# Kernel tuning notes

Hardware: AMD Instinct MI355X
Metric: run time of the kernel (lower is better)

Reference implementation:

```python
import jax, jax.numpy as jnp
import numpy as np

N_CIR, N_DIS, D, H = 585, 88, 128, 8
E_CC, E_DD = 20000, 3000
EPS = 1e-16


def _gcn(x, src, dst, ew, W, b, N):
    # PyG GCNConv: add self-loops (weight 1), symmetric normalization, x @ W, scatter-add, + bias
    loop = jnp.arange(N)
    s = jnp.concatenate([src, loop])
    d = jnp.concatenate([dst, loop])
    w = jnp.concatenate([ew, jnp.ones((N,), ew.dtype)])
    deg = jax.ops.segment_sum(w, d, num_segments=N)
    dinv = jnp.where(deg > 0, jax.lax.rsqrt(deg), 0.0)
    norm = dinv[s] * w * dinv[d]                      # [E+N]
    h = x @ W                                         # [N,D]
    out = jax.ops.segment_sum(h[s] * norm[:, None], d, num_segments=N)
    return out + b


def _gat(x, src, dst, ea, W, a_src, a_dst, a_edge, We, b, N):
    # PyG GATConv(heads=H, concat=False, edge_dim=1): self-loops with mean edge_attr fill,
    # leaky_relu attention logits, segment softmax over destination, mean over heads, + bias
    loop = jnp.arange(N)
    s = jnp.concatenate([src, loop])
    d = jnp.concatenate([dst, loop])
    ea = jnp.concatenate([ea, jnp.broadcast_to(ea.mean(0, keepdims=True), (N, ea.shape[1]))], 0)
    h = (x @ W).reshape(N, H, D)                      # [N,H,D]
    e = (ea @ We).reshape(-1, H, D)                   # [E+N,H,D]
    alpha = (h * a_src).sum(-1)[s] + (h * a_dst).sum(-1)[d] + (e * a_edge).sum(-1)
    alpha = jax.nn.leaky_relu(alpha, 0.2)             # [E+N,H]
    amax = jax.ops.segment_max(alpha, d, num_segments=N)
    ex = jnp.exp(alpha - amax[d])
    den = jax.ops.segment_sum(ex, d, num_segments=N)
    alpha = ex / (den[d] + EPS)
    out = jax.ops.segment_sum(h[s] * alpha[:, :, None], d, num_segments=N)  # [N,H,D]
    return out.mean(1) + b


def _branch(x, edges, mat, gw1, gb1, aw, asrc, adst, aedge, awe, ab, gw2, gb2, N):
    src, dst = edges[0], edges[1]
    ew = mat[src, dst]                                # gather edge weights from dense matrix
    f1 = jax.nn.relu(_gcn(x, src, dst, ew, gw1, gb1, N))
    att = jax.nn.relu(_gat(f1, src, dst, ew[:, None], aw, asrc, adst, aedge, awe, ab, N))
    f2 = jax.nn.relu(_gcn(att, src, dst, ew, gw2, gb2, N))
    return f1, f2


def _cnn(f1, f2, Wk, b):
    # Conv2d(2,256,(128,1)) over [1,2,128,N] == per-node GEMM over (2,128) then view/transpose
    Xv = jnp.stack([f1.T, f2.T])                      # [2,D,N]
    return jnp.einsum('ock,ckn->no', Wk[..., 0], Xv) + b  # [N,256]


def setup_inputs():
    ks = jax.random.split(jax.random.key(0), 24)
    rn = lambda i, sh, s=1.0: jax.random.normal(ks[i], sh, jnp.float32) * s
    w = 0.08  # ~glorot scale for fan-in 128
    return {
        'x_cir': rn(0, (N_CIR, D)),
        'x_dis': rn(1, (N_DIS, D)),
        'cc_matrix': jax.random.uniform(ks[2], (N_CIR, N_CIR), jnp.float32),
        'dd_matrix': jax.random.uniform(ks[3], (N_DIS, N_DIS), jnp.float32),
        'gcn_c1_w': rn(4, (D, D), w), 'gcn_c1_b': jnp.zeros((D,), jnp.float32),
        'gat_c_w': rn(5, (D, H * D), w), 'gat_c_asrc': rn(6, (H, D), w),
        'gat_c_adst': rn(7, (H, D), w), 'gat_c_aedge': rn(8, (H, D), w),
        'gat_c_we': rn(9, (1, H * D), w), 'gat_c_b': jnp.zeros((D,), jnp.float32),
        'gcn_c2_w': rn(10, (D, D), w), 'gcn_c2_b': jnp.zeros((D,), jnp.float32),
        'gcn_d1_w': rn(11, (D, D), w), 'gcn_d1_b': jnp.zeros((D,), jnp.float32),
        'gat_d_w': rn(12, (D, H * D), w), 'gat_d_asrc': rn(13, (H, D), w),
        'gat_d_adst': rn(14, (H, D), w), 'gat_d_aedge': rn(15, (H, D), w),
        'gat_d_we': rn(16, (1, H * D), w), 'gat_d_b': jnp.zeros((D,), jnp.float32),
        'gcn_d2_w': rn(17, (D, D), w), 'gcn_d2_b': jnp.zeros((D,), jnp.float32),
        'conv_c_w': rn(18, (256, 2, D, 1), w), 'conv_c_b': jnp.zeros((256,), jnp.float32),
        'conv_d_w': rn(19, (256, 2, D, 1), w), 'conv_d_b': jnp.zeros((256,), jnp.float32),
        'cc_edges': jax.random.randint(ks[20], (2, E_CC), 0, N_CIR),
        'dd_edges': jax.random.randint(ks[21], (2, E_DD), 0, N_DIS),
    }


def reference(x_cir, x_dis, cc_matrix, dd_matrix,
              gcn_c1_w, gcn_c1_b, gat_c_w, gat_c_asrc, gat_c_adst, gat_c_aedge, gat_c_we, gat_c_b,
              gcn_c2_w, gcn_c2_b,
              gcn_d1_w, gcn_d1_b, gat_d_w, gat_d_asrc, gat_d_adst, gat_d_aedge, gat_d_we, gat_d_b,
              gcn_d2_w, gcn_d2_b,
              conv_c_w, conv_c_b, conv_d_w, conv_d_b,
              cc_edges, dd_edges):
    c1, c2 = _branch(x_cir, cc_edges, cc_matrix, gcn_c1_w, gcn_c1_b, gat_c_w, gat_c_asrc,
                     gat_c_adst, gat_c_aedge, gat_c_we, gat_c_b, gcn_c2_w, gcn_c2_b, N_CIR)
    d1, d2 = _branch(x_dis, dd_edges, dd_matrix, gcn_d1_w, gcn_d1_b, gat_d_w, gat_d_asrc,
                     gat_d_adst, gat_d_aedge, gat_d_we, gat_d_b, gcn_d2_w, gcn_d2_b, N_DIS)
    cir_fea = _cnn(c1, c2, conv_c_w, conv_c_b)        # [585,256]
    dis_fea = _cnn(d1, d2, conv_d_w, conv_d_b)        # [88,256]
    return cir_fea @ dis_fea.T, cir_fea, dis_fea
```

## Files before the change

### kernel.cpp

```cpp
#include <hip/hip_runtime.h>

constexpr int NCIR = 585;
constexpr int NDIS = 88;
constexpr int NT   = NCIR + NDIS;
constexpr int DIM  = 128;
constexpr int NH   = 8;
constexpr int ECC  = 20000;
constexpr int EDD  = 3000;
constexpr int ET   = ECC + EDD;
constexpr int CO   = 256;
constexpr int CAP  = 256;
constexpr int F1C  = (NCIR + 3) / 4;
constexpr int F1D  = (NDIS + 3) / 4;
constexpr int NG   = F1C + F1D;
constexpr int GBK  = (ET + 255) / 256;
constexpr int GEMB = (NT + 1) / 2;

__device__ __forceinline__ int decode_cnt(unsigned raw){
  return (int)(raw >= 0xA0000000u ? raw - 0xAAAAAAAAu : raw);
}

struct P {
  const float *x_c, *x_d, *mat_c, *mat_d;
  const float *g1w_c, *g1b_c, *aw_c, *as_c, *ad_c, *ae_c, *we_c, *ab_c, *g2w_c, *g2b_c;
  const float *g1w_d, *g1b_d, *aw_d, *as_d, *ad_d, *ae_d, *we_d, *ab_d, *g2w_d, *g2b_d;
  const float *cw_c, *cb_c, *cw_d, *cb_d;
  const int *csrc, *cdst, *dsrc, *ddst;
  float *hs, *hd, *h, *f1, *hg, *fill_w, *psc, *psd, *wdeg, *wdall;
  unsigned *cnt;
  int *fill_s;
  float *out_score, *out_cir, *out_dis;
};

__global__ __launch_bounds__(256) void k_gg(P p){
  __shared__ float r0[256], r1[256];
  int b = blockIdx.x, t = threadIdx.x;
  if (b < GBK){
    int e = b * 256 + t;
    float wc = 0.0f, wdv = 0.0f;
    if (e < ET){
      float w; int s, d;
      if (e < ECC){
        s = p.csrc[e]; d = p.cdst[e];
        w = p.mat_c[s * NCIR + d]; wc = w;
      } else {
        int el = e - ECC;
        s = NCIR + p.dsrc[el]; d = NCIR + p.ddst[el];
        w = p.mat_d[(s - NCIR) * NDIS + (d - NCIR)]; wdv = w;
      }
      int pos = decode_cnt(atomicAdd(&p.cnt[d], 1u));
      if (pos < CAP){
        p.fill_s[d * CAP + pos] = s;
        p.fill_w[d * CAP + pos] = w;
      }
      atomicAdd(&p.wdeg[d], w);
    }
    r0[t] = wc; r1[t] = wdv;
    __syncthreads();
    for (int st = 128; st; st >>= 1){
      if (t < st){ r0[t] += r0[t + st]; r1[t] += r1[t + st]; }
      __syncthreads();
    }
    if (t == 0){ p.psc[b] = r0[0]; p.psd[b] = r1[0]; }
  } else if (b < GBK + GEMB){
    int ub = (b - GBK) * 2;
    int n = t >> 7, k = t & 127;
    int u = ub + n;
    bool ok = u < NT;
    if (ok){
      int br = u >= NCIR;
      r0[n * DIM + k] = br ? p.x_d[(u - NCIR) * DIM + k] : p.x_c[u * DIM + k];
    }
    __syncthreads();
    if (ok){
      const float* W = (u >= NCIR) ? p.g1w_d : p.g1w_c;
      float acc = 0.0f;
      #pragma unroll 8
      for (int c = 0; c < DIM; ++c) acc += r0[n * DIM + c] * W[c * DIM + k];
      p.h[u * DIM + k] = acc;
    }
  } else {
    int brn = b - (GBK + GEMB);
    const float* We = brn ? p.we_d : p.we_c;
    const float* Ae = brn ? p.ae_d : p.ae_c;
    int hh = t >> 5, l = t & 31;
    float v = 0.0f;
    #pragma unroll
    for (int q = l; q < DIM; q += 32) v += We[hh * DIM + q] * Ae[hh * DIM + q];
    #pragma unroll
    for (int off = 16; off; off >>= 1) v += __shfl_down(v, off, 32);
    if (l == 0) p.wdall[brn * NH + hh] = v;
  }
}

__global__ __launch_bounds__(256) void k_aggproj(P p){
  __shared__ int   deg4[4];
  __shared__ float dv4[4];
  __shared__ int   s4[4][CAP];
  __shared__ float nrm4[4][CAP];
  __shared__ __align__(16) float apart[8][DIM];
  __shared__ float a_sh[4][DIM];
  __shared__ float wred[4][8];
  int b = blockIdx.x, t = threadIdx.x;
  int ng = b >> 2, ct = b & 3;
  int base, count, br;
  if (ng < F1C){ base = ng * 4; count = min(4, NCIR - base); br = 0; }
  else { base = NCIR + (ng - F1C) * 4; count = 4; br = 1; }
  if (t < 4){
    if (t < count){
      int u = base + t;
      deg4[t] = min(decode_cnt(p.cnt[u]), CAP);
      dv4[t]  = rsqrtf(1.0f + p.wdeg[u]);
    } else deg4[t] = 0;
  }
  __syncthreads();
  for (int idx = t; idx < 4 * CAP; idx += 256){
    int nn = idx >> 8, j = idx & (CAP - 1);
    if (j < deg4[nn]){
      int u = base + nn;
      int s = p.fill_s[u * CAP + j];
      s4[nn][j] = s;
      nrm4[nn][j] = rsqrtf(1.0f + p.wdeg[s]) * p.fill_w[u * CAP + j] * dv4[nn];
    }
  }
  __syncthreads();
  {
    int slot = t >> 5, lane = t & 31;
    int nn = slot >> 1, jp = slot & 1;
    float4 acc4 = {0.f, 0.f, 0.f, 0.f};
    if (nn < count){
      if (jp == 0){
        int u = base + nn;
        float sc = dv4[nn] * dv4[nn];
        const float4* B14 = (const float4*)(br ? p.g1b_d : p.g1b_c);
        const float4* h4  = (const float4*)(p.h + (size_t)u * DIM);
        float4 bb = B14[lane], hv = h4[lane];
        acc4.x = bb.x + hv.x * sc; acc4.y = bb.y + hv.y * sc;
        acc4.z = bb.z + hv.z * sc; acc4.w = bb.w + hv.w * sc;
      }
      int deg = deg4[nn];
      #pragma unroll 4
      for (int j = jp; j < deg; j += 2){
        const float4* hr = (const float4*)(p.h + (size_t)s4[nn][j] * DIM);
        float w = nrm4[nn][j];
        float4 hv = hr[lane];
        acc4.x += hv.x * w; acc4.y += hv.y * w;
        acc4.z += hv.z * w; acc4.w += hv.w * w;
      }
    }
    ((float4*)apart[slot])[lane] = acc4;
  }
  __syncthreads();
  {
    int n2 = t >> 7, k = t & 127;
    for (int r = 0; r < 2; ++r){
      int nn = n2 + r * 2;
      float sum = apart[nn * 2][k] + apart[nn * 2 + 1][k];
      if (nn < count && ct == 0) p.f1[(size_t)(base + nn) * DIM + k] = sum;
      a_sh[nn][k] = (nn < count) ? fmaxf(sum, 0.0f) : 0.0f;
    }
  }
  __syncthreads();
  const float* W = (br ? p.aw_d : p.aw_c) + ct * 256 + t;
  float acc[4] = {0.f, 0.f, 0.f, 0.f};
  #pragma unroll 4
  for (int c = 0; c < DIM; ++c){
    float w = W[c * 1024];
    acc[0] += a_sh[0][c] * w; acc[1] += a_sh[1][c] * w;
    acc[2] += a_sh[2][c] * w; acc[3] += a_sh[3][c] * w;
  }
  int col = ct * 256 + t;
  for (int n = 0; n < count; ++n)
    p.hg[(size_t)(base + n) * 1024 + col] = acc[n];
  const float* As = br ? p.as_d : p.as_c;
  const float* Ad = br ? p.ad_d : p.ad_c;
  float av = As[col], dw = Ad[col];
  int w = t >> 6;
  #pragma unroll
  for (int n = 0; n < 4; ++n){
    float sdot = acc[n] * av, ddot = acc[n] * dw;
    #pragma unroll
    for (int off = 32; off; off >>= 1){
      sdot += __shfl_down(sdot, off, 64);
      ddot += __shfl_down(ddot, off, 64);
    }
    if ((t & 63) == 0){ wred[w][n * 2] = sdot; wred[w][n * 2 + 1] = ddot; }
  }
  __syncthreads();
  if (t < 16){
    int g = t >> 3, v = t & 7, n = v >> 1, isd = v & 1;
    if (n < count){
      float sum = wred[g * 2][v] + wred[g * 2 + 1][v];
      float* dst = isd ? p.hd : p.hs;
      dst[(base + n) * NH + ct * 2 + g] = sum;
    }
  }
}

__global__ __launch_bounds__(256) void k_att(P p){
  __shared__ float den_sh[NH], hd_sh[NH], inv_sh[NH], wself_sh[NH], wd_sh[NH];
  __shared__ float slw_sh;
  __shared__ int   s_all[CAP];
  __shared__ float w_all[CAP];
  __shared__ float alpha_all[CAP * NH];
  __shared__ __align__(16) float hacc[NH][DIM];
  __shared__ float attv[DIM];
  __shared__ float part[2][DIM];
  int d = blockIdx.x, t = threadIdx.x;
  int g = t >> 7, k = t & 127;
  int br = d >= NCIR;
  int wv = t >> 6, lane64 = t & 63;
  if (t < NH){
    den_sh[t] = 0.0f;
    hd_sh[t]  = p.hd[d * NH + t];
    wd_sh[t]  = p.wdall[br * NH + t];
  }
  if (wv == 0){
    const float* ps = br ? p.psd : p.psc;
    float v = (lane64 < GBK ? ps[lane64] : 0.0f) + (lane64 + 64 < GBK ? ps[lane64 + 64] : 0.0f);
    #pragma unroll
    for (int off = 32; off; off >>= 1) v += __shfl_down(v, off, 64);
    if (lane64 == 0) slw_sh = v / (br ? (float)EDD : (float)ECC);
  }
  int deg = min(decode_cnt(p.cnt[d]), CAP);
  for (int j = t; j < deg; j += 256){
    s_all[j] = p.fill_s[d * CAP + j];
    w_all[j] = p.fill_w[d * CAP + j];
  }
  __syncthreads();
  int bound = deg * NH;
  for (int i0 = 0; i0 < bound; i0 += 256){
    int idx = i0 + t;
    float ex = 0.0f;
    if (idx < bound){
      int j = idx >> 3, hh = idx & 7;
      float a = p.hs[s_all[j] * NH + hh] + hd_sh[hh] + w_all[j] * wd_sh[hh];
      a = a > 0.0f ? a : 0.2f * a;
      ex = expf(a);
      alpha_all[idx] = ex;
    }
    float v = ex;
    v += __shfl_xor(v, 8, 64);
    v += __shfl_xor(v, 16, 64);
    v += __shfl_xor(v, 32, 64);
    if (lane64 < 8) atomicAdd(&den_sh[lane64], v);
  }
  __syncthreads();
  if (t < NH){
    float a = p.hs[d * NH + t] + hd_sh[t] + slw_sh * wd_sh[t];
    a = a > 0.0f ? a : 0.2f * a;
    float ex = expf(a);
    float inv = 1.0f / (den_sh[t] + ex + 1e-16f) * 0.125f;
    inv_sh[t] = inv;
    wself_sh[t] = ex * inv;
  }
  __syncthreads();
  {
    int hh = t >> 5, lane = t & 31;
    float sc = inv_sh[hh];
    const float4* rd = (const float4*)(p.hg + (size_t)d * 1024 + hh * DIM);
    float ws = wself_sh[hh];
    float4 v = rd[lane];
    float4 acc4 = {ws * v.x, ws * v.y, ws * v.z, ws * v.w};
    #pragma unroll 4
    for (int jj = 0; jj < deg; ++jj){
      const float4* r = (const float4*)(p.hg + (size_t)s_all[jj] * 1024 + hh * DIM);
      float a = alpha_all[jj * NH + hh] * sc;
      float4 hv = r[lane];
      acc4.x += a * hv.x; acc4.y += a * hv.y;
      acc4.z += a * hv.z; acc4.w += a * hv.w;
    }
    ((float4*)hacc[hh])[lane] = acc4;
  }
  __syncthreads();
  {
    float s0 = hacc[g * 4 + 0][k] + hacc[g * 4 + 1][k]
             + hacc[g * 4 + 2][k] + hacc[g * 4 + 3][k];
    part[g][k] = s0;
  }
  __syncthreads();
  if (g == 0)
    attv[k] = fmaxf((br ? p.ab_d : p.ab_c)[k] + part[0][k] + part[1][k], 0.0f);
  __syncthreads();
  const float* W = br ? p.g2w_d : p.g2w_c;
  float h2 = 0.0f;
  #pragma unroll 8
  for (int c = g * 64; c < g * 64 + 64; ++c) h2 += attv[c] * W[c * DIM + k];
  part[g][k] = h2;
  __syncthreads();
  if (g == 0) p.h[d * DIM + k] = part[0][k] + part[1][k];
}

__global__ __launch_bounds__(256) void k_fuse2(P p){
  __shared__ int   s_all[CAP];
  __shared__ float nrm_all[CAP];
  __shared__ __align__(16) float red[8][DIM];
  __shared__ __align__(16) float s12[2 * DIM];
  int u = blockIdx.x, t = threadIdx.x;
  int br = u >= NCIR;
  float* out = br ? p.out_dis + (size_t)(u - NCIR) * CO
                  : p.out_cir + (size_t)u * CO;
  int deg = min(decode_cnt(p.cnt[u]), CAP);
  float dvu = rsqrtf(1.0f + p.wdeg[u]);
  for (int j = t; j < deg; j += 256){
    int s = p.fill_s[u * CAP + j];
    s_all[j] = s;
    nrm_all[j] = rsqrtf(1.0f + p.wdeg[s]) * p.fill_w[u * CAP + j] * dvu;
  }
  __syncthreads();
  {
    int slot = t >> 5, lane = t & 31;
    float4 acc4 = {0.f, 0.f, 0.f, 0.f};
    if (slot == 0){
      const float4* B24 = (const float4*)(br ? p.g2b_d : p.g2b_c);
      const float4* h4  = (const float4*)(p.h + (size_t)u * DIM);
      float sc = dvu * dvu;
      float4 bb = B24[lane], hv = h4[lane];
      acc4.x = bb.x + hv.x * sc; acc4.y = bb.y + hv.y * sc;
      acc4.z = bb.z + hv.z * sc; acc4.w = bb.w + hv.w * sc;
    }
    #pragma unroll 4
    for (int j = slot; j < deg; j += 8){
      const float4* hr = (const float4*)(p.h + (size_t)s_all[j] * DIM);
      float w = nrm_all[j];
      float4 hv = hr[lane];
      acc4.x += hv.x * w; acc4.y += hv.y * w;
      acc4.z += hv.z * w; acc4.w += hv.w * w;
    }
    ((float4*)red[slot])[lane] = acc4;
  }
  __syncthreads();
  if (t < DIM){
    float sum = red[0][t] + red[1][t] + red[2][t] + red[3][t]
              + red[4][t] + red[5][t] + red[6][t] + red[7][t];
    s12[DIM + t] = fmaxf(sum, 0.0f);
    s12[t]       = fmaxf(p.f1[(size_t)u * DIM + t], 0.0f);
  }
  __syncthreads();
  const float4* W4 = (const float4*)((br ? p.cw_d : p.cw_c) + (size_t)t * 2 * DIM);
  const float4* sv = (const float4*)s12;
  float acc = (br ? p.cb_d : p.cb_c)[t];
  #pragma unroll 8
  for (int q = 0; q < 64; ++q){
    float4 w = W4[q], s = sv[q];
    acc += w.x * s.x + w.y * s.y + w.z * s.z + w.w * s.w;
  }
  out[t] = acc;
}

__global__ void k_final(P p){
  __shared__ __align__(16) float ci[CO];
  __shared__ float fin[2][NDIS];
  int i = blockIdx.x, t = threadIdx.x;
  ci[t] = p.out_cir[(size_t)i * CO + t];
  __syncthreads();
  int half = t >> 7, j = t & 127;
  if (j < NDIS){
    const float4* dr = (const float4*)(p.out_dis + (size_t)j * CO + half * DIM);
    const float4* cc = (const float4*)(ci + half * DIM);
    float acc = 0.0f;
    #pragma unroll 8
    for (int q = 0; q < 32; ++q){
      float4 a = cc[q], b = dr[q];
      acc += a.x * b.x + a.y * b.y + a.z * b.z + a.w * b.w;
    }
    fin[half][j] = acc;
  }
  __syncthreads();
  if (t < NDIS) p.out_score[(size_t)i * NDIS + t] = fin[0][t] + fin[1][t];
}

extern "C" void kernel_launch(void* const* d_in, const int* in_sizes, int n_in,
                              void* d_out, int out_size, void* d_ws, size_t ws_size,
                              hipStream_t stream){
  P p;
  typedef const float* F;
  p.x_c   = (F)d_in[0];  p.x_d   = (F)d_in[1];
  p.mat_c = (F)d_in[2];  p.mat_d = (F)d_in[3];
  p.g1w_c = (F)d_in[4];  p.g1b_c = (F)d_in[5];
  p.aw_c  = (F)d_in[6];  p.as_c  = (F)d_in[7];  p.ad_c = (F)d_in[8];
  p.ae_c  = (F)d_in[9];  p.we_c  = (F)d_in[10]; p.ab_c = (F)d_in[11];
  p.g2w_c = (F)d_in[12]; p.g2b_c = (F)d_in[13];
  p.g1w_d = (F)d_in[14]; p.g1b_d = (F)d_in[15];
  p.aw_d  = (F)d_in[16]; p.as_d  = (F)d_in[17]; p.ad_d = (F)d_in[18];
  p.ae_d  = (F)d_in[19]; p.we_d  = (F)d_in[20]; p.ab_d = (F)d_in[21];
  p.g2w_d = (F)d_in[22]; p.g2b_d = (F)d_in[23];
  p.cw_c  = (F)d_in[24]; p.cb_c  = (F)d_in[25];
  p.cw_d  = (F)d_in[26]; p.cb_d  = (F)d_in[27];
  const int* cc_edges = (const int*)d_in[28];
  const int* dd_edges = (const int*)d_in[29];
  p.csrc = cc_edges;  p.cdst = cc_edges + ECC;
  p.dsrc = dd_edges;  p.ddst = dd_edges + EDD;

  float* out = (float*)d_out;
  p.out_score = out;
  p.out_cir   = out + NCIR * NDIS;
  p.out_dis   = p.out_cir + NCIR * CO;

  float* w = (float*)d_ws;
  auto alloc = [&](size_t n){ float* q = w; w += n; return q; };
  p.wdeg   = alloc(676);
  p.cnt    = (unsigned*)alloc(676);
  p.psc    = alloc(92);
  p.psd    = alloc(92);
  p.wdall  = alloc(16);
  p.hs     = alloc((size_t)NT * NH);
  p.hd     = alloc((size_t)NT * NH);
  p.h      = alloc((size_t)NT * DIM);
  p.f1     = alloc((size_t)NT * DIM);
  p.hg     = alloc((size_t)NT * 1024);
  p.fill_w = alloc((size_t)NT * CAP);
  p.fill_s = (int*)alloc((size_t)NT * CAP);

  k_gg     <<<GBK + GEMB + 2, 256, 0, stream>>>(p);
  k_aggproj<<<NG * 4,         256, 0, stream>>>(p);
  k_att    <<<NT,             256, 0, stream>>>(p);
  k_fuse2  <<<NT,             256, 0, stream>>>(p);
  k_final  <<<NCIR,           256, 0, stream>>>(p);
}
```

Before: 192.3 us.

## Fuse final score GEMM into fuse2 via inter-block counter, batch first GEMM

Removes the separate k_final launch. Disease-node blocks are reordered to run first in the fused kernel and bump a global completion counter, and circRNA blocks spin-wait on that counter before computing their score row from the conv output still held in registers. The first-layer x@W in k_gg now handles four nodes per block, so each loaded weight value is reused for two rows. The head reduction in k_att is also collapsed into a single pass with one fewer barrier. The spin-wait assumes the disease blocks are scheduled first, risking a stall or deadlock if they are not resident, and it relies on the workspace counter being reset before each call.

```diff
diff --git a/kernel.cpp b/kernel.cpp
--- a/kernel.cpp
+++ b/kernel.cpp
@@ -14,7 +14,7 @@
 constexpr int F1D  = (NDIS + 3) / 4;
 constexpr int NG   = F1C + F1D;
 constexpr int GBK  = (ET + 255) / 256;
-constexpr int GEMB = (NT + 1) / 2;
+constexpr int GEMB4 = (NT + 3) / 4;
 
 __device__ __forceinline__ int decode_cnt(unsigned raw){
   return (int)(raw >= 0xA0000000u ? raw - 0xAAAAAAAAu : raw);
@@ -27,15 +27,17 @@
   const float *cw_c, *cb_c, *cw_d, *cb_d;
   const int *csrc, *cdst, *dsrc, *ddst;
   float *hs, *hd, *h, *f1, *hg, *fill_w, *psc, *psd, *wdeg, *wdall;
-  unsigned *cnt;
+  unsigned *cnt, *done;
   int *fill_s;
   float *out_score, *out_cir, *out_dis;
 };
 
 __global__ __launch_bounds__(256) void k_gg(P p){
-  __shared__ float r0[256], r1[256];
+  __shared__ float sbuf[512];
   int b = blockIdx.x, t = threadIdx.x;
   if (b < GBK){
+    float* r0 = sbuf;
+    float* r1 = sbuf + 256;
     int e = b * 256 + t;
     float wc = 0.0f, wdv = 0.0f;
     if (e < ET){
@@ -62,25 +64,43 @@
       __syncthreads();
     }
     if (t == 0){ p.psc[b] = r0[0]; p.psd[b] = r1[0]; }
-  } else if (b < GBK + GEMB){
-    int ub = (b - GBK) * 2;
-    int n = t >> 7, k = t & 127;
-    int u = ub + n;
-    bool ok = u < NT;
-    if (ok){
-      int br = u >= NCIR;
-      r0[n * DIM + k] = br ? p.x_d[(u - NCIR) * DIM + k] : p.x_c[u * DIM + k];
+  } else if (b < GBK + GEMB4){
+    int base = (b - GBK) * 4;
+    for (int idx = t; idx < 512; idx += 256){
+      int n = idx >> 7, k2 = idx & 127;
+      int u = base + n;
+      float v = 0.0f;
+      if (u < NT) v = (u >= NCIR) ? p.x_d[(u - NCIR) * DIM + k2]
+                                  : p.x_c[u * DIM + k2];
+      sbuf[idx] = v;
     }
     __syncthreads();
-    if (ok){
-      const float* W = (u >= NCIR) ? p.g1w_d : p.g1w_c;
-      float acc = 0.0f;
+    int k = t & 127, np = t >> 7;
+    int u0 = base + 2 * np, u1 = u0 + 1;
+    bool mixed = (base < NCIR) && (base + 3 >= NCIR);
+    if (!mixed){
+      const float* W = (base >= NCIR) ? p.g1w_d : p.g1w_c;
+      float a0 = 0.0f, a1 = 0.0f;
       #pragma unroll 8
-      for (int c = 0; c < DIM; ++c) acc += r0[n * DIM + c] * W[c * DIM + k];
-      p.h[u * DIM + k] = acc;
+      for (int c = 0; c < DIM; ++c){
+        float wv = W[c * DIM + k];
+        a0 += sbuf[2 * np * DIM + c] * wv;
+        a1 += sbuf[(2 * np + 1) * DIM + c] * wv;
+      }
+      if (u0 < NT) p.h[(size_t)u0 * DIM + k] = a0;
+      if (u1 < NT) p.h[(size_t)u1 * DIM + k] = a1;
+    } else {
+      for (int r = 0; r < 2; ++r){
+        int u = base + 2 * np + r;
+        const float* W = (u >= NCIR) ? p.g1w_d : p.g1w_c;
+        float a = 0.0f;
+        #pragma unroll 8
+        for (int c = 0; c < DIM; ++c) a += sbuf[(2 * np + r) * DIM + c] * W[c * DIM + k];
+        p.h[(size_t)u * DIM + k] = a;
+      }
     }
   } else {
-    int brn = b - (GBK + GEMB);
+    int brn = b - (GBK + GEMB4);
     const float* We = brn ? p.we_d : p.we_c;
     const float* Ae = brn ? p.ae_d : p.ae_c;
     int hh = t >> 5, l = t & 31;
@@ -273,14 +293,12 @@
     ((float4*)hacc[hh])[lane] = acc4;
   }
   __syncthreads();
-  {
-    float s0 = hacc[g * 4 + 0][k] + hacc[g * 4 + 1][k]
-             + hacc[g * 4 + 2][k] + hacc[g * 4 + 3][k];
-    part[g][k] = s0;
-  }
-  __syncthreads();
-  if (g == 0)
-    attv[k] = fmaxf((br ? p.ab_d : p.ab_c)[k] + part[0][k] + part[1][k], 0.0f);
+  if (g == 0){
+    float s0 = 0.0f;
+    #pragma unroll
+    for (int hh = 0; hh < NH; ++hh) s0 += hacc[hh][k];
+    attv[k] = fmaxf((br ? p.ab_d : p.ab_c)[k] + s0, 0.0f);
+  }
   __syncthreads();
   const float* W = br ? p.g2w_d : p.g2w_c;
   float h2 = 0.0f;
@@ -291,15 +309,16 @@
   if (g == 0) p.h[d * DIM + k] = part[0][k] + part[1][k];
 }
 
-__global__ __launch_bounds__(256) void k_fuse2(P p){
+__global__ __launch_bounds__(256) void k_fuse2f(P p){
   __shared__ int   s_all[CAP];
   __shared__ float nrm_all[CAP];
   __shared__ __align__(16) float red[8][DIM];
   __shared__ __align__(16) float s12[2 * DIM];
-  int u = blockIdx.x, t = threadIdx.x;
-  int br = u >= NCIR;
-  float* out = br ? p.out_dis + (size_t)(u - NCIR) * CO
-                  : p.out_cir + (size_t)u * CO;
+  int b = blockIdx.x, t = threadIdx.x;
+  int br = b < NDIS;
+  int u  = br ? NCIR + b : b - NDIS;
+  float* out = br ? p.out_dis + (size_t)b * CO
+                  : p.out_cir + (size_t)(b - NDIS) * CO;
   int deg = min(decode_cnt(p.cnt[u]), CAP);
   float dvu = rsqrtf(1.0f + p.wdeg[u]);
   for (int j = t; j < deg; j += 256){
@@ -346,28 +365,39 @@
     acc += w.x * s.x + w.y * s.y + w.z * s.z + w.w * s.w;
   }
   out[t] = acc;
-}
-
-__global__ void k_final(P p){
-  __shared__ __align__(16) float ci[CO];
-  __shared__ float fin[2][NDIS];
-  int i = blockIdx.x, t = threadIdx.x;
-  ci[t] = p.out_cir[(size_t)i * CO + t];
+  if (br){
+    __syncthreads();
+    if (t == 0){
+      __threadfence();
+      atomicAdd(p.done, 1u);
+    }
+    return;
+  }
+  float* ci  = &red[0][0];
+  float* fin = ci + CO;
+  ci[t] = acc;
+  if (t == 0){
+    while (decode_cnt(__hip_atomic_load(p.done, __ATOMIC_ACQUIRE,
+                                        __HIP_MEMORY_SCOPE_AGENT)) < NDIS){
+      __builtin_amdgcn_s_sleep(16);
+    }
+  }
   __syncthreads();
   int half = t >> 7, j = t & 127;
   if (j < NDIS){
     const float4* dr = (const float4*)(p.out_dis + (size_t)j * CO + half * DIM);
     const float4* cc = (const float4*)(ci + half * DIM);
-    float acc = 0.0f;
+    float a2 = 0.0f;
     #pragma unroll 8
     for (int q = 0; q < 32; ++q){
-      float4 a = cc[q], b = dr[q];
-      acc += a.x * b.x + a.y * b.y + a.z * b.z + a.w * b.w;
-    }
-    fin[half][j] = acc;
-  }
-  __syncthreads();
-  if (t < NDIS) p.out_score[(size_t)i * NDIS + t] = fin[0][t] + fin[1][t];
+      float4 a = cc[q], bb = dr[q];
+      a2 += a.x * bb.x + a.y * bb.y + a.z * bb.z + a.w * bb.w;
+    }
+    fin[half * NDIS + j] = a2;
+  }
+  __syncthreads();
+  if (t < NDIS)
+    p.out_score[(size_t)(b - NDIS) * NDIS + t] = fin[t] + fin[NDIS + t];
 }
 
 extern "C" void kernel_launch(void* const* d_in, const int* in_sizes, int n_in,
@@ -401,6 +431,7 @@
   auto alloc = [&](size_t n){ float* q = w; w += n; return q; };
   p.wdeg   = alloc(676);
   p.cnt    = (unsigned*)alloc(676);
+  p.done   = (unsigned*)alloc(4);
   p.psc    = alloc(92);
   p.psd    = alloc(92);
   p.wdall  = alloc(16);
@@ -412,9 +443,8 @@
   p.fill_w = alloc((size_t)NT * CAP);
   p.fill_s = (int*)alloc((size_t)NT * CAP);
 
-  k_gg     <<<GBK + GEMB + 2, 256, 0, stream>>>(p);
-  k_aggproj<<<NG * 4,         256, 0, stream>>>(p);
-  k_att    <<<NT,             256, 0, stream>>>(p);
-  k_fuse2  <<<NT,             256, 0, stream>>>(p);
-  k_final  <<<NCIR,           256, 0, stream>>>(p);
-}
+  k_gg     <<<GBK + GEMB4 + 2, 256, 0, stream>>>(p);
+  k_aggproj<<<NG * 4,          256, 0, stream>>>(p);
+  k_att    <<<NT,              256, 0, stream>>>(p);
+  k_fuse2f <<<NT,              256, 0, stream>>>(p);
+}
```

After: 215.2 us. 1.12x slower.
